# Performance work log

Measured on AMD Instinct MI355X. Metric: run time of the kernel, lower is better.

## Reference

```python
import jax, jax.numpy as jnp
import numpy as np

N_HEAD = 32
N_QUERY_GROUPS = 8
HEAD_SIZE = 128
N_EMBD = 4096


def apply_rope(x, cos, sin):
    # x: [B, H, T, D]; cos/sin: [T, D] (rotary_percentage = 1.0 so D = head_size)
    d = x.shape[-1]
    x1, x2 = x[..., : d // 2], x[..., d // 2:]
    rotated = jnp.concatenate([-x2, x1], axis=-1)
    return x * cos + rotated * sin


def setup_inputs() -> dict:
    key = jax.random.key(0)
    k1, k2, k3, k4, k5 = jax.random.split(key, 5)
    B, T = 1, 2048
    x = jax.random.normal(k1, (B, T, N_EMBD), dtype=jnp.float32)
    # realistic rope angles
    theta = 10000.0 ** (-jnp.arange(0, HEAD_SIZE // 2, dtype=jnp.float32) * 2.0 / HEAD_SIZE)
    ang = jnp.arange(T, dtype=jnp.float32)[:, None] * theta[None, :]
    ang = jnp.concatenate([ang, ang], axis=-1)  # [T, HEAD_SIZE]
    cos, sin = jnp.cos(ang), jnp.sin(ang)
    qkv_dim = (N_HEAD + 2 * N_QUERY_GROUPS) * HEAD_SIZE  # 6144
    w_attn = jax.random.normal(k2, (qkv_dim, N_EMBD), dtype=jnp.float32) * (N_EMBD ** -0.5)
    w_proj = jax.random.normal(k3, (N_EMBD, N_HEAD * HEAD_SIZE), dtype=jnp.float32) * ((N_HEAD * HEAD_SIZE) ** -0.5)
    return {"x": x, "cos": cos, "sin": sin, "w_attn": w_attn, "w_proj": w_proj}


def reference(x, cos, sin, w_attn, w_proj):
    B, T, C = x.shape
    G, hs = N_QUERY_GROUPS, HEAD_SIZE
    q_per_kv = N_HEAD // G  # 4
    total_qkv = q_per_kv + 2

    qkv = jnp.einsum('btc,oc->bto', x, w_attn)  # [B, T, 6144]
    qkv = qkv.reshape(B, T, G, total_qkv, hs).transpose(0, 2, 3, 1, 4)  # [B, G, total, T, hs]
    q = qkv[:, :, :q_per_kv]              # [B, G, qpk, T, hs]
    k = qkv[:, :, q_per_kv:q_per_kv + 1]  # [B, G, 1,   T, hs]
    v = qkv[:, :, q_per_kv + 1:]          # [B, G, 1,   T, hs]

    # GQA expand to per-query heads, then flatten head dims
    k = jnp.broadcast_to(k, (B, G, q_per_kv, T, hs))
    v = jnp.broadcast_to(v, (B, G, q_per_kv, T, hs))
    q = q.reshape(B, N_HEAD, T, hs)
    k = k.reshape(B, N_HEAD, T, hs)
    v = v.reshape(B, N_HEAD, T, hs)

    # rotary_percentage = 1.0 -> rope over full head dim
    q = apply_rope(q, cos, sin)
    k = apply_rope(k, cos, sin)

    scale = 1.0 / jnp.sqrt(jnp.float32(hs))
    scores = jnp.einsum('bhqd,bhkd->bhqk', q, k) * scale  # [B, H, T, T]
    causal = jnp.tril(jnp.ones((T, T), dtype=bool))
    scores = jnp.where(causal, scores, jnp.finfo(scores.dtype).min)
    attn = jax.nn.softmax(scores, axis=-1)
    y = jnp.einsum('bhqk,bhkd->bhqd', attn, v)  # [B, H, T, hs]
    y = y.transpose(0, 2, 1, 3).reshape(B, T, N_HEAD * hs)
    return jnp.einsum('bto,co->btc', y, w_proj)  # [B, T, C]
```

## Files before the change

### kernel.cpp

```cpp
#include <hip/hip_runtime.h>
#include <hip/hip_bf16.h>

typedef __attribute__((ext_vector_type(8))) short short8;
typedef __attribute__((ext_vector_type(4))) float f32x4;

__device__ inline unsigned short f2bf(float f) {
  __hip_bfloat16 h = __float2bfloat16(f);
  return *reinterpret_cast<unsigned short*>(&h);
}
__device__ inline float bf2f(unsigned short u) {
  union { unsigned u; float f; } v; v.u = ((unsigned)u) << 16;
  return v.f;
}

#define GLOAD_LDS16(g, l)                                          \
  __builtin_amdgcn_global_load_lds(                                \
      (const __attribute__((address_space(1))) void*)(g),          \
      (__attribute__((address_space(3))) void*)(l), 16, 0, 0)

#define MFMA16(a, b, c) __builtin_amdgcn_mfma_f32_16x16x32_bf16((a), (b), (c), 0, 0, 0)

#define LGKM0()                                              \
  asm volatile("s_waitcnt lgkmcnt(0)" ::: "memory");         \
  __builtin_amdgcn_sched_barrier(0);

__global__ void cvt3(const float* __restrict__ x, const float* __restrict__ wa,
                     const float* __restrict__ wp, unsigned short* __restrict__ Xb,
                     unsigned short* __restrict__ Wa, unsigned short* __restrict__ Wp) {
  const int N_X = 1048576, N_WA = 3145728;
  const int TOT = 6291456;
  for (int i = blockIdx.x * 256 + threadIdx.x; i < TOT; i += gridDim.x * 256) {
    const float* src; unsigned short* dst; int off;
    if (i < N_X)            { src = x;  dst = Xb; off = i; }
    else if (i < N_X + N_WA){ src = wa; dst = Wa; off = i - N_X; }
    else                    { src = wp; dst = Wp; off = i - N_X - N_WA; }
    const float4* p = (const float4*)src + (size_t)off * 2;
    float4 a = p[0], b = p[1];
    short8 v;
    v[0] = f2bf(a.x); v[1] = f2bf(a.y); v[2] = f2bf(a.z); v[3] = f2bf(a.w);
    v[4] = f2bf(b.x); v[5] = f2bf(b.y); v[6] = f2bf(b.z); v[7] = f2bf(b.w);
    *((short8*)dst + off) = v;
  }
}

__global__ __launch_bounds__(512, 2)
void gemm_qkv(const unsigned short* __restrict__ A, const unsigned short* __restrict__ B,
              unsigned short* __restrict__ C, int M, int N, int K) {
  __shared__ __align__(16) unsigned short lds[2][448 * 64];
  const int t = threadIdx.x, lane = t & 63, w = t >> 6;
  const int wm = w >> 1, wn = w & 1;
  const int r16 = lane & 15, kg = lane >> 4;
  const int bm = blockIdx.x & 7, bn = blockIdx.x >> 3;
  const int NT = K >> 6;
  const int sr = lane >> 3, sch = lane & 7;
  const unsigned short* Ag = A + (size_t)(bm * 256) * K;
  const unsigned short* Bg = B + (size_t)(bn * 192) * K;

  auto stA = [&](int kt, int j, int b) {
    int rl = j * 64 + w * 8 + sr, sc = sch ^ (rl & 7);
    GLOAD_LDS16(Ag + (size_t)rl * K + kt * 64 + sc * 8, &lds[b][(j * 64 + w * 8) * 64]);
  };
  auto stB = [&](int kt, int j, int b) {
    int rl = j * 64 + w * 8 + sr, sc = sch ^ (rl & 7);
    GLOAD_LDS16(Bg + (size_t)rl * K + kt * 64 + sc * 8, &lds[b][(256 + j * 64 + w * 8) * 64]);
  };
  auto lda = [&](int b, int m, int kk) -> short8 {
    int row = wm * 64 + m * 16 + r16, ch = (kk * 4 + kg) ^ (row & 7);
    return *(const short8*)__builtin_assume_aligned(&lds[b][row * 64 + ch * 8], 16);
  };
  auto ldb = [&](int b, int n, int kk) -> short8 {
    int row = wn * 96 + n * 16 + r16, ch = (kk * 4 + kg) ^ (row & 7);
    return *(const short8*)__builtin_assume_aligned(&lds[b][(256 + row) * 64 + ch * 8], 16);
  };

  f32x4 acc[4][6] = {};
  short8 af[4][2], bb[6][2];

#pragma unroll
  for (int j = 0; j < 4; ++j) stA(0, j, 0);
#pragma unroll
  for (int j = 0; j < 3; ++j) stB(0, j, 0);
#pragma unroll
  for (int j = 0; j < 4; ++j) stA(1, j, 1);
  asm volatile("s_waitcnt vmcnt(4)" ::: "memory");
  __builtin_amdgcn_sched_barrier(0);
  __builtin_amdgcn_s_barrier();

  for (int kt = 0; kt < NT; ++kt) {
    const int b = kt & 1;
    const bool pf1 = kt + 1 < NT, pf2 = kt + 2 < NT;

    if (pf1) { stB(kt + 1, 0, b ^ 1); stB(kt + 1, 1, b ^ 1); stB(kt + 1, 2, b ^ 1); }
#pragma unroll
    for (int m = 0; m < 4; ++m) { af[m][0] = lda(b, m, 0); af[m][1] = lda(b, m, 1); }
#pragma unroll
    for (int n = 0; n < 2; ++n) { bb[n][0] = ldb(b, n, 0); bb[n][1] = ldb(b, n, 1); }
    __builtin_amdgcn_s_barrier();
    LGKM0();
    __builtin_amdgcn_s_setprio(1);
#pragma unroll
    for (int m = 0; m < 4; ++m)
#pragma unroll
      for (int n = 0; n < 2; ++n)
#pragma unroll
        for (int kk = 0; kk < 2; ++kk) acc[m][n] = MFMA16(af[m][kk], bb[n][kk], acc[m][n]);
    __builtin_amdgcn_s_setprio(0);
    __builtin_amdgcn_s_barrier();

    if (pf2) { stA(kt + 2, 0, b); stA(kt + 2, 1, b); stA(kt + 2, 2, b); stA(kt + 2, 3, b); }
#pragma unroll
    for (int n = 2; n < 6; ++n) { bb[n][0] = ldb(b, n, 0); bb[n][1] = ldb(b, n, 1); }
    __builtin_amdgcn_s_barrier();
    LGKM0();
    __builtin_amdgcn_s_setprio(1);
#pragma unroll
    for (int m = 0; m < 4; ++m)
#pragma unroll
      for (int n = 2; n < 6; ++n)
#pragma unroll
        for (int kk = 0; kk < 2; ++kk) acc[m][n] = MFMA16(af[m][kk], bb[n][kk], acc[m][n]);
    __builtin_amdgcn_s_setprio(0);
    if (pf1) {
      if (pf2) asm volatile("s_waitcnt vmcnt(4)" ::: "memory");
      else     asm volatile("s_waitcnt vmcnt(0)" ::: "memory");
      __builtin_amdgcn_sched_barrier(0);
      __builtin_amdgcn_s_barrier();
    }
  }

#pragma unroll
  for (int m = 0; m < 4; ++m)
#pragma unroll
    for (int n = 0; n < 6; ++n)
#pragma unroll
      for (int j = 0; j < 4; ++j) {
        int row = bm * 256 + wm * 64 + m * 16 + kg * 4 + j;
        int col = bn * 192 + wn * 96 + n * 16 + r16;
        C[(size_t)row * N + col] = f2bf(acc[m][n][j]);
      }
}

__global__ __launch_bounds__(512, 1)
void gemm_proj(const unsigned short* __restrict__ A, const unsigned short* __restrict__ B,
               float* __restrict__ C, int M, int N, int K) {
  __shared__ __align__(16) unsigned short lds[2][384 * 64];
  const int t = threadIdx.x, lane = t & 63, w = t >> 6;
  const int wm = w >> 2, wn = w & 3;
  const int r16 = lane & 15, kg = lane >> 4;
  const int bm = blockIdx.x & 15, bn = blockIdx.x >> 4;
  const int NT = K >> 6;
  const int sr = lane >> 3, sch = lane & 7;
  const unsigned short* Ag = A + (size_t)(bm * 128) * K;
  const unsigned short* Bg = B + (size_t)(bn * 256) * K;

  auto stA = [&](int kt, int j, int b) {
    int rl = j * 64 + w * 8 + sr, sc = sch ^ (rl & 7);
    GLOAD_LDS16(Ag + (size_t)rl * K + kt * 64 + sc * 8, &lds[b][(j * 64 + w * 8) * 64]);
  };
  auto stB = [&](int kt, int j, int b) {
    int rl = j * 64 + w * 8 + sr, sc = sch ^ (rl & 7);
    GLOAD_LDS16(Bg + (size_t)rl * K + kt * 64 + sc * 8, &lds[b][(128 + j * 64 + w * 8) * 64]);
  };
  auto lda = [&](int b, int m, int kk) -> short8 {
    int row = wm * 64 + m * 16 + r16, ch = (kk * 4 + kg) ^ (row & 7);
    return *(const short8*)__builtin_assume_aligned(&lds[b][row * 64 + ch * 8], 16);
  };
  auto ldb = [&](int b, int n, int kk) -> short8 {
    int row = wn * 64 + n * 16 + r16, ch = (kk * 4 + kg) ^ (row & 7);
    return *(const short8*)__builtin_assume_aligned(&lds[b][(128 + row) * 64 + ch * 8], 16);
  };

  f32x4 acc[4][4] = {};
  short8 af[4][2], bb[4][2];

#pragma unroll
  for (int j = 0; j < 2; ++j) stA(0, j, 0);
#pragma unroll
  for (int j = 0; j < 4; ++j) stB(0, j, 0);
#pragma unroll
  for (int j = 0; j < 2; ++j) stA(1, j, 1);
#pragma unroll
  for (int j = 0; j < 4; ++j) stB(1, j, 1);
  asm volatile("s_waitcnt vmcnt(6)" ::: "memory");
  __builtin_amdgcn_sched_barrier(0);
  __builtin_amdgcn_s_barrier();

  for (int kt = 0; kt < NT; ++kt) {
    const int b = kt & 1;
    const bool pf1 = kt + 1 < NT, pf2 = kt + 2 < NT;

#pragma unroll
    for (int m = 0; m < 2; ++m) { af[m][0] = lda(b, m, 0); af[m][1] = lda(b, m, 1); }
#pragma unroll
    for (int n = 0; n < 2; ++n) { bb[n][0] = ldb(b, n, 0); bb[n][1] = ldb(b, n, 1); }
    __builtin_amdgcn_s_barrier();
    LGKM0();
    __builtin_amdgcn_s_setprio(1);
#pragma unroll
    for (int m = 0; m < 2; ++m)
#pragma unroll
      for (int n = 0; n < 2; ++n)
#pragma unroll
        for (int kk = 0; kk < 2; ++kk) acc[m][n] = MFMA16(af[m][kk], bb[n][kk], acc[m][n]);
    __builtin_amdgcn_s_setprio(0);
    __builtin_amdgcn_s_barrier();

#pragma unroll
    for (int n = 2; n < 4; ++n) { bb[n][0] = ldb(b, n, 0); bb[n][1] = ldb(b, n, 1); }
    __builtin_amdgcn_s_barrier();
    LGKM0();
    __builtin_amdgcn_s_setprio(1);
#pragma unroll
    for (int m = 0; m < 2; ++m)
#pragma unroll
      for (int n = 2; n < 4; ++n)
#pragma unroll
        for (int kk = 0; kk < 2; ++kk) acc[m][n] = MFMA16(af[m][kk], bb[n][kk], acc[m][n]);
    __builtin_amdgcn_s_setprio(0);
    __builtin_amdgcn_s_barrier();

#pragma unroll
    for (int m = 2; m < 4; ++m) { af[m][0] = lda(b, m, 0); af[m][1] = lda(b, m, 1); }
    if (pf2) { stB(kt + 2, 0, b); stB(kt + 2, 1, b); stB(kt + 2, 2, b); stB(kt + 2, 3, b); }
    __builtin_amdgcn_s_barrier();
    LGKM0();
    __builtin_amdgcn_s_setprio(1);
#pragma unroll
    for (int m = 2; m < 4; ++m)
#pragma unroll
      for (int n = 2; n < 4; ++n)
#pragma unroll
        for (int kk = 0; kk < 2; ++kk) acc[m][n] = MFMA16(af[m][kk], bb[n][kk], acc[m][n]);
    __builtin_amdgcn_s_setprio(0);
    __builtin_amdgcn_s_barrier();

    if (pf2) { stA(kt + 2, 0, b); stA(kt + 2, 1, b); }
    __builtin_amdgcn_s_setprio(1);
#pragma unroll
    for (int m = 2; m < 4; ++m)
#pragma unroll
      for (int n = 0; n < 2; ++n)
#pragma unroll
        for (int kk = 0; kk < 2; ++kk) acc[m][n] = MFMA16(af[m][kk], bb[n][kk], acc[m][n]);
    __builtin_amdgcn_s_setprio(0);
    if (pf1) {
      if (pf2) asm volatile("s_waitcnt vmcnt(6)" ::: "memory");
      else     asm volatile("s_waitcnt vmcnt(0)" ::: "memory");
      __builtin_amdgcn_sched_barrier(0);
      __builtin_amdgcn_s_barrier();
    }
  }

#pragma unroll
  for (int m = 0; m < 4; ++m)
#pragma unroll
    for (int n = 0; n < 4; ++n)
#pragma unroll
      for (int j = 0; j < 4; ++j) {
        int row = bm * 128 + wm * 64 + m * 16 + kg * 4 + j;
        int col = bn * 256 + wn * 64 + n * 16 + r16;
        C[(size_t)row * N + col] = acc[m][n][j];
      }
}

__global__ void rope_tv(const unsigned short* __restrict__ qkv,
                        const float* __restrict__ cosb, const float* __restrict__ sinb,
                        unsigned short* __restrict__ Q, unsigned short* __restrict__ K,
                        unsigned short* __restrict__ Vt) {
  __shared__ __align__(16) unsigned short tile[64][136];
  const int bid = blockIdx.x;
  if (bid < 20480) {
    int pair = bid * 4 + (threadIdx.x >> 6);
    int l = threadIdx.x & 63;
    int t = pair / 40, slot = pair - t * 40;
    const unsigned short* src;
    unsigned short* dst;
    float scale;
    if (slot < 32) {
      int g = slot >> 2, j = slot & 3;
      src = qkv + (size_t)t * 6144 + g * 768 + j * 128;
      dst = Q + ((size_t)slot * 2048 + t) * 128;
      scale = 0.08838834764831845f;
    } else {
      int g = slot - 32;
      src = qkv + (size_t)t * 6144 + g * 768 + 512;
      dst = K + ((size_t)g * 2048 + t) * 128;
      scale = 1.0f;
    }
    float x1 = bf2f(src[l]), x2 = bf2f(src[64 + l]);
    float c1 = cosb[t * 128 + l], s1 = sinb[t * 128 + l];
    float c2 = cosb[t * 128 + 64 + l], s2 = sinb[t * 128 + 64 + l];
    dst[l]      = f2bf((x1 * c1 - x2 * s1) * scale);
    dst[64 + l] = f2bf((x2 * c2 + x1 * s2) * scale);
  } else {
    int b2 = bid - 20480;
    int g = b2 >> 5, t0 = (b2 & 31) * 64;
    int th = threadIdx.x;
    int r = th >> 2, c0 = (th & 3) * 32;
    const unsigned short* src = qkv + (size_t)(t0 + r) * 6144 + g * 768 + 640 + c0;
#pragma unroll
    for (int i = 0; i < 4; ++i)
      *(short8*)&tile[r][c0 + i * 8] = *(const short8*)(src + i * 8);
    __syncthreads();
    int d = th >> 1, tc = (th & 1) * 32;
    unsigned short* dst = Vt + (size_t)(g * 128 + d) * 2048 + t0 + tc;
#pragma unroll
    for (int j = 0; j < 32; ++j) dst[j] = tile[tc + j][d];
  }
}

__global__ __launch_bounds__(256, 2)
void flash_attn(const unsigned short* __restrict__ Q, const unsigned short* __restrict__ K,
                const unsigned short* __restrict__ Vt, unsigned short* __restrict__ Y) {
  __shared__ __align__(16) unsigned short Ksm[2][64 * 128];
  __shared__ __align__(16) unsigned short Vsm[2][128 * 64];

  const int h = blockIdx.y, g = h >> 2;
  const int t = threadIdx.x, lane = t & 63, w = t >> 6;
  const int r16 = lane & 15, kg = lane >> 4;
  const bool odd = kg & 1;
  const bool hi = kg >> 1;
  const bool useswap = odd ^ hi;

  const unsigned short* Kg = K + (size_t)g * 2048 * 128;
  const unsigned short* Vg = Vt + (size_t)g * 128 * 2048;

  const int krl = lane >> 4, kc = lane & 15;
  const int vrl = lane >> 3, vc = lane & 7;

  auto stage = [&](int kvs, int b) {
#pragma unroll
    for (int i = 0; i < 4; ++i) {
      int row = w * 16 + i * 4 + krl;
      int sc = kc ^ (row & 7);
      GLOAD_LDS16(Kg + (size_t)(kvs + row) * 128 + sc * 8,
                  &Ksm[b][(w * 16 + i * 4) * 128]);
    }
#pragma unroll
    for (int i = 0; i < 4; ++i) {
      int d = w * 32 + i * 8 + vrl;
      int sc = vc ^ (d & 7);
      GLOAD_LDS16(Vg + (size_t)d * 2048 + kvs + sc * 8,
                  &Vsm[b][(w * 32 + i * 8) * 64]);
    }
  };

  auto process = [&](int q0) {
    short8 qf[4];
    const unsigned short* qrow = Q + ((size_t)h * 2048 + q0 + w * 16 + r16) * 128;
#pragma unroll
    for (int kk = 0; kk < 4; ++kk) qf[kk] = *(const short8*)(qrow + kk * 32 + kg * 8);

    f32x4 o[8] = {};
    float mrow = -1e30f, lrow = 0.f;
    const int qg = q0 + w * 16 + r16;
    const int nt = q0 / 64 + 1;

    __syncthreads();
    stage(0, 0);

    for (int kt = 0; kt < nt; ++kt) {
      const int b = kt & 1;
      const int kv0 = kt * 64;
      __syncthreads();
      if (kt + 1 < nt) stage((kt + 1) * 64, b ^ 1);

      f32x4 s[4] = {};
      __builtin_amdgcn_s_setprio(1);
#pragma unroll
      for (int n = 0; n < 4; ++n) {
        int kr = n * 16 + r16;
#pragma unroll
        for (int kk = 0; kk < 4; ++kk) {
          short8 kf = *(const short8*)__builtin_assume_aligned(
              &Ksm[b][kr * 128 + ((kk * 32 + kg * 8) ^ ((kr & 7) << 3))], 16);
          s[n] = __builtin_amdgcn_mfma_f32_16x16x32_bf16(kf, qf[kk], s[n], 0, 0, 0);
        }
      }
      __builtin_amdgcn_s_setprio(0);

      if (kv0 + 63 > q0 + w * 16) {
#pragma unroll
        for (int n = 0; n < 4; ++n)
#pragma unroll
          for (int j = 0; j < 4; ++j)
            if (kv0 + n * 16 + kg * 4 + j > qg) s[n][j] = -1e30f;
      }

      float rmax = -1e30f;
#pragma unroll
      for (int n = 0; n < 4; ++n)
#pragma unroll
        for (int j = 0; j < 4; ++j) rmax = fmaxf(rmax, s[n][j]);
      rmax = fmaxf(rmax, __shfl_xor(rmax, 16));
      rmax = fmaxf(rmax, __shfl_xor(rmax, 32));

      if (__builtin_amdgcn_ballot_w64(rmax > mrow)) {
        float mnew = fmaxf(mrow, rmax);
        float fac = __expf(mrow - mnew);
        mrow = mnew;
        lrow *= fac;
        float fj[4];
#pragma unroll
        for (int j = 0; j < 4; ++j) fj[j] = __shfl(fac, kg * 4 + j);
#pragma unroll
        for (int f = 0; f < 8; ++f)
#pragma unroll
          for (int j = 0; j < 4; ++j) o[f][j] *= fj[j];
      }

      float p[4][4];
      float rs = 0.f;
#pragma unroll
      for (int n = 0; n < 4; ++n)
#pragma unroll
        for (int j = 0; j < 4; ++j) {
          p[n][j] = __expf(s[n][j] - mrow);
          rs += p[n][j];
        }
      rs += __shfl_xor(rs, 16);
      rs += __shfl_xor(rs, 32);
      lrow += rs;

      unsigned bpk[4][2], xpk[4][2];
#pragma unroll
      for (int n = 0; n < 4; ++n)
#pragma unroll
        for (int i = 0; i < 2; ++i)
          bpk[n][i] = (unsigned)f2bf(p[n][2 * i]) | ((unsigned)f2bf(p[n][2 * i + 1]) << 16);
#pragma unroll
      for (int n = 0; n < 4; ++n)
#pragma unroll
        for (int i = 0; i < 2; ++i) xpk[n][i] = __shfl_xor(bpk[n][i], 16);

      unsigned pl[4][2], ph[4][2];
#pragma unroll
      for (int n = 0; n < 4; ++n)
#pragma unroll
        for (int i = 0; i < 2; ++i) {
          pl[n][i] = odd ? xpk[n][i] : bpk[n][i];
          ph[n][i] = odd ? bpk[n][i] : xpk[n][i];
        }

      short8 pa[2];
#pragma unroll
      for (int kk = 0; kk < 2; ++kk) {
        unsigned kp0 = hi ? pl[2 * kk + 1][0] : pl[2 * kk][0];
        unsigned kp1 = hi ? pl[2 * kk + 1][1] : pl[2 * kk][1];
        unsigned kp2 = hi ? ph[2 * kk + 1][0] : ph[2 * kk][0];
        unsigned kp3 = hi ? ph[2 * kk + 1][1] : ph[2 * kk][1];
        unsigned sd0 = hi ? pl[2 * kk][0] : pl[2 * kk + 1][0];
        unsigned sd1 = hi ? pl[2 * kk][1] : pl[2 * kk + 1][1];
        unsigned sd2 = hi ? ph[2 * kk][0] : ph[2 * kk + 1][0];
        unsigned sd3 = hi ? ph[2 * kk][1] : ph[2 * kk + 1][1];
        unsigned g0 = __shfl_xor(sd0, 32), g1 = __shfl_xor(sd1, 32);
        unsigned g2 = __shfl_xor(sd2, 32), g3 = __shfl_xor(sd3, 32);
        union { unsigned u[4]; short8 v; } pu;
        pu.u[0] = useswap ? g0 : kp0;
        pu.u[1] = useswap ? g1 : kp1;
        pu.u[2] = useswap ? g2 : kp2;
        pu.u[3] = useswap ? g3 : kp3;
        pa[kk] = pu.v;
      }

      __builtin_amdgcn_s_setprio(1);
#pragma unroll
      for (int kk = 0; kk < 2; ++kk) {
#pragma unroll
        for (int f = 0; f < 8; ++f) {
          int d = f * 16 + r16;
          short8 vf = *(const short8*)__builtin_assume_aligned(
              &Vsm[b][d * 64 + ((kk * 32 + kg * 8) ^ ((d & 7) << 3))], 16);
          o[f] = __builtin_amdgcn_mfma_f32_16x16x32_bf16(pa[kk], vf, o[f], 0, 0, 0);
        }
      }
      __builtin_amdgcn_s_setprio(0);
    }

    float inv = 1.f / lrow;
    float invj[4];
#pragma unroll
    for (int j = 0; j < 4; ++j) invj[j] = __shfl(inv, kg * 4 + j);
#pragma unroll
    for (int j = 0; j < 4; ++j) {
      int row = q0 + w * 16 + kg * 4 + j;
      unsigned short* yr = Y + (size_t)row * 4096 + h * 128;
#pragma unroll
      for (int f = 0; f < 8; ++f) yr[f * 16 + r16] = f2bf(o[f][j] * invj[j]);
    }
  };

  const int pr = blockIdx.x;
  process(pr * 64);
  process((31 - pr) * 64);
}

extern "C" void kernel_launch(void* const* d_in, const int* in_sizes, int n_in,
                              void* d_out, int out_size, void* d_ws, size_t ws_size,
                              hipStream_t stream) {
  const float* x      = (const float*)d_in[0];
  const float* cosb   = (const float*)d_in[1];
  const float* sinb   = (const float*)d_in[2];
  const float* w_attn = (const float*)d_in[3];
  const float* w_proj = (const float*)d_in[4];
  float* out = (float*)d_out;

  char* ws = (char*)d_ws;
  const size_t MB = 1024 * 1024;
  unsigned short* Xb  = (unsigned short*)(ws);
  unsigned short* Wa  = (unsigned short*)(ws + 16 * MB);
  unsigned short* Wp  = (unsigned short*)(ws + 112 * MB);
  unsigned short* Qb  = (unsigned short*)(ws + 32 * MB);
  unsigned short* Kb  = (unsigned short*)(ws + 48 * MB);
  unsigned short* Vt  = (unsigned short*)(ws + 52 * MB);
  unsigned short* qkv = (unsigned short*)(ws + 64 * MB);
  unsigned short* Yb  = (unsigned short*)(ws + 88 * MB);

  cvt3<<<2048, 256, 0, stream>>>(x, w_attn, w_proj, Xb, Wa, Wp);
  gemm_qkv<<<256, 512, 0, stream>>>(Xb, Wa, qkv, 2048, 6144, 4096);
  rope_tv<<<20736, 256, 0, stream>>>(qkv, cosb, sinb, Qb, Kb, Vt);
  flash_attn<<<dim3(16, 32), 256, 0, stream>>>(Qb, Kb, Vt, Yb);
  gemm_proj<<<256, 512, 0, stream>>>(Yb, Wp, out, 2048, 4096, 4096);
}
```

Baseline: 313.5 us.

## Retile proj GEMM to 256x128 and switch attention softmax to exp2 with lazy rescale

The output-projection GEMM tile changes from 128x256 to 256x128, with 2x4 waves each covering 64x64. The K-loop is restructured into two MFMA phases, with B prefetched one stage ahead and A two stages ahead. In attention, log2(e) is folded into the Q scale so the softmax can use exp2. The running max is rescaled only when the new max exceeds the old one by more than 8, which cuts rescale work but lets unnormalised values grow up to 2^8 in fp32/bf16.

```diff
diff --git a/kernel.cpp b/kernel.cpp
--- a/kernel.cpp
+++ b/kernel.cpp
@@ -145,13 +145,13 @@
                float* __restrict__ C, int M, int N, int K) {
   __shared__ __align__(16) unsigned short lds[2][384 * 64];
   const int t = threadIdx.x, lane = t & 63, w = t >> 6;
-  const int wm = w >> 2, wn = w & 3;
+  const int wm = w >> 1, wn = w & 1;
   const int r16 = lane & 15, kg = lane >> 4;
-  const int bm = blockIdx.x & 15, bn = blockIdx.x >> 4;
+  const int bm = blockIdx.x & 7, bn = blockIdx.x >> 3;
   const int NT = K >> 6;
   const int sr = lane >> 3, sch = lane & 7;
-  const unsigned short* Ag = A + (size_t)(bm * 128) * K;
-  const unsigned short* Bg = B + (size_t)(bn * 256) * K;
+  const unsigned short* Ag = A + (size_t)(bm * 256) * K;
+  const unsigned short* Bg = B + (size_t)(bn * 128) * K;
 
   auto stA = [&](int kt, int j, int b) {
     int rl = j * 64 + w * 8 + sr, sc = sch ^ (rl & 7);
@@ -159,7 +159,7 @@
   };
   auto stB = [&](int kt, int j, int b) {
     int rl = j * 64 + w * 8 + sr, sc = sch ^ (rl & 7);
-    GLOAD_LDS16(Bg + (size_t)rl * K + kt * 64 + sc * 8, &lds[b][(128 + j * 64 + w * 8) * 64]);
+    GLOAD_LDS16(Bg + (size_t)rl * K + kt * 64 + sc * 8, &lds[b][(256 + j * 64 + w * 8) * 64]);
   };
   auto lda = [&](int b, int m, int kk) -> short8 {
     int row = wm * 64 + m * 16 + r16, ch = (kk * 4 + kg) ^ (row & 7);
@@ -167,21 +167,19 @@
   };
   auto ldb = [&](int b, int n, int kk) -> short8 {
     int row = wn * 64 + n * 16 + r16, ch = (kk * 4 + kg) ^ (row & 7);
-    return *(const short8*)__builtin_assume_aligned(&lds[b][(128 + row) * 64 + ch * 8], 16);
+    return *(const short8*)__builtin_assume_aligned(&lds[b][(256 + row) * 64 + ch * 8], 16);
   };
 
   f32x4 acc[4][4] = {};
   short8 af[4][2], bb[4][2];
 
 #pragma unroll
-  for (int j = 0; j < 2; ++j) stA(0, j, 0);
-#pragma unroll
-  for (int j = 0; j < 4; ++j) stB(0, j, 0);
-#pragma unroll
-  for (int j = 0; j < 2; ++j) stA(1, j, 1);
-#pragma unroll
-  for (int j = 0; j < 4; ++j) stB(1, j, 1);
-  asm volatile("s_waitcnt vmcnt(6)" ::: "memory");
+  for (int j = 0; j < 4; ++j) stA(0, j, 0);
+#pragma unroll
+  for (int j = 0; j < 2; ++j) stB(0, j, 0);
+#pragma unroll
+  for (int j = 0; j < 4; ++j) stA(1, j, 1);
+  asm volatile("s_waitcnt vmcnt(4)" ::: "memory");
   __builtin_amdgcn_sched_barrier(0);
   __builtin_amdgcn_s_barrier();
 
@@ -189,15 +187,16 @@
     const int b = kt & 1;
     const bool pf1 = kt + 1 < NT, pf2 = kt + 2 < NT;
 
-#pragma unroll
-    for (int m = 0; m < 2; ++m) { af[m][0] = lda(b, m, 0); af[m][1] = lda(b, m, 1); }
+    if (pf1) { stB(kt + 1, 0, b ^ 1); stB(kt + 1, 1, b ^ 1); }
+#pragma unroll
+    for (int m = 0; m < 4; ++m) { af[m][0] = lda(b, m, 0); af[m][1] = lda(b, m, 1); }
 #pragma unroll
     for (int n = 0; n < 2; ++n) { bb[n][0] = ldb(b, n, 0); bb[n][1] = ldb(b, n, 1); }
     __builtin_amdgcn_s_barrier();
     LGKM0();
     __builtin_amdgcn_s_setprio(1);
 #pragma unroll
-    for (int m = 0; m < 2; ++m)
+    for (int m = 0; m < 4; ++m)
 #pragma unroll
       for (int n = 0; n < 2; ++n)
 #pragma unroll
@@ -205,46 +204,21 @@
     __builtin_amdgcn_s_setprio(0);
     __builtin_amdgcn_s_barrier();
 
+    if (pf2) { stA(kt + 2, 0, b); stA(kt + 2, 1, b); stA(kt + 2, 2, b); stA(kt + 2, 3, b); }
 #pragma unroll
     for (int n = 2; n < 4; ++n) { bb[n][0] = ldb(b, n, 0); bb[n][1] = ldb(b, n, 1); }
     __builtin_amdgcn_s_barrier();
     LGKM0();
     __builtin_amdgcn_s_setprio(1);
 #pragma unroll
-    for (int m = 0; m < 2; ++m)
+    for (int m = 0; m < 4; ++m)
 #pragma unroll
       for (int n = 2; n < 4; ++n)
-#pragma unroll
-        for (int kk = 0; kk < 2; ++kk) acc[m][n] = MFMA16(af[m][kk], bb[n][kk], acc[m][n]);
-    __builtin_amdgcn_s_setprio(0);
-    __builtin_amdgcn_s_barrier();
-
-#pragma unroll
-    for (int m = 2; m < 4; ++m) { af[m][0] = lda(b, m, 0); af[m][1] = lda(b, m, 1); }
-    if (pf2) { stB(kt + 2, 0, b); stB(kt + 2, 1, b); stB(kt + 2, 2, b); stB(kt + 2, 3, b); }
-    __builtin_amdgcn_s_barrier();
-    LGKM0();
-    __builtin_amdgcn_s_setprio(1);
-#pragma unroll
-    for (int m = 2; m < 4; ++m)
-#pragma unroll
-      for (int n = 2; n < 4; ++n)
-#pragma unroll
-        for (int kk = 0; kk < 2; ++kk) acc[m][n] = MFMA16(af[m][kk], bb[n][kk], acc[m][n]);
-    __builtin_amdgcn_s_setprio(0);
-    __builtin_amdgcn_s_barrier();
-
-    if (pf2) { stA(kt + 2, 0, b); stA(kt + 2, 1, b); }
-    __builtin_amdgcn_s_setprio(1);
-#pragma unroll
-    for (int m = 2; m < 4; ++m)
-#pragma unroll
-      for (int n = 0; n < 2; ++n)
 #pragma unroll
         for (int kk = 0; kk < 2; ++kk) acc[m][n] = MFMA16(af[m][kk], bb[n][kk], acc[m][n]);
     __builtin_amdgcn_s_setprio(0);
     if (pf1) {
-      if (pf2) asm volatile("s_waitcnt vmcnt(6)" ::: "memory");
+      if (pf2) asm volatile("s_waitcnt vmcnt(4)" ::: "memory");
       else     asm volatile("s_waitcnt vmcnt(0)" ::: "memory");
       __builtin_amdgcn_sched_barrier(0);
       __builtin_amdgcn_s_barrier();
@@ -257,8 +231,8 @@
     for (int n = 0; n < 4; ++n)
 #pragma unroll
       for (int j = 0; j < 4; ++j) {
-        int row = bm * 128 + wm * 64 + m * 16 + kg * 4 + j;
-        int col = bn * 256 + wn * 64 + n * 16 + r16;
+        int row = bm * 256 + wm * 64 + m * 16 + kg * 4 + j;
+        int col = bn * 128 + wn * 64 + n * 16 + r16;
         C[(size_t)row * N + col] = acc[m][n][j];
       }
 }
@@ -280,7 +254,7 @@
       int g = slot >> 2, j = slot & 3;
       src = qkv + (size_t)t * 6144 + g * 768 + j * 128;
       dst = Q + ((size_t)slot * 2048 + t) * 128;
-      scale = 0.08838834764831845f;
+      scale = 0.08838834764831845f * 1.4426950408889634f;
     } else {
       int g = slot - 32;
       src = qkv + (size_t)t * 6144 + g * 768 + 512;
@@ -395,9 +369,9 @@
       rmax = fmaxf(rmax, __shfl_xor(rmax, 16));
       rmax = fmaxf(rmax, __shfl_xor(rmax, 32));
 
-      if (__builtin_amdgcn_ballot_w64(rmax > mrow)) {
+      if (__builtin_amdgcn_ballot_w64(rmax > mrow + 8.0f)) {
         float mnew = fmaxf(mrow, rmax);
-        float fac = __expf(mrow - mnew);
+        float fac = exp2f(mrow - mnew);
         mrow = mnew;
         lrow *= fac;
         float fj[4];
@@ -415,7 +389,7 @@
       for (int n = 0; n < 4; ++n)
 #pragma unroll
         for (int j = 0; j < 4; ++j) {
-          p[n][j] = __expf(s[n][j] - mrow);
+          p[n][j] = exp2f(s[n][j] - mrow);
           rs += p[n][j];
         }
       rs += __shfl_xor(rs, 16);
```

Measured after the change: 315.5 us. No clear change (+0.6%).
